# Kernel tuning notes

Measured on AMD Instinct MI355X. Metric: run time of the kernel, lower is better.

## Reference

```python
import jax, jax.numpy as jnp
import numpy as np

C = 8            # feat_channel
B, K, H, W = 8, 32, 128, 128
CW = (C + 2) * C + C + C * C + C + C + 1  # 169


def setup_inputs() -> dict:
    key = jax.random.key(0)
    k1, k2, k3, k4, k5 = jax.random.split(key, 5)
    seg_feat = jax.random.normal(k1, (B, C, H, W), jnp.float32)
    conv_weight = jax.random.normal(k2, (B, CW, H, W), jnp.float32) * 0.1
    mask = jax.random.randint(k3, (B, K), 0, 2).astype(jnp.int32)
    ind = jax.random.randint(k4, (B, K), 0, H * W).astype(jnp.int64)
    target = jax.random.uniform(k5, (B, K, H, W), jnp.float32)
    return {"seg_feat": seg_feat, "conv_weight": conv_weight, "mask": mask,
            "ind": ind, "target": target}


def reference(seg_feat, conv_weight, mask, ind, target):
    b, c, h, w = seg_feat.shape
    k = ind.shape[1]
    # gather_feature(conv_weight, ind, use_transform=True): [B,CW,H,W] -> [B,HW,CW] -> gather -> [B,K,CW]
    cw = conv_weight.reshape(b, -1, h * w).transpose(0, 2, 1)
    weight = jnp.take_along_axis(cw, ind[:, :, None], axis=1)  # [B,K,CW]

    sizes = [(c + 2) * c, c, c * c, c, c, 1]
    splits = np.cumsum(sizes)[:-1]
    c1w, c1b, c2w, c2b, c3w, c3b = jnp.split(weight, splits, axis=-1)
    c1w = c1w.reshape(b, k, c, c + 2)   # per-object 1x1 conv weights
    c2w = c2w.reshape(b, k, c, c)
    c3w = c3w.reshape(b, k, 1, c)

    x = (ind % w).astype(jnp.float32)
    y = (ind // w).astype(jnp.float32)
    y_grid, x_grid = jnp.meshgrid(jnp.arange(h, dtype=jnp.float32),
                                  jnp.arange(w, dtype=jnp.float32), indexing='ij')
    x_rel = (x_grid[None, None] - x[:, :, None, None]) / w   # [B,K,H,W]
    y_rel = (y_grid[None, None] - y[:, :, None, None]) / h

    feat = jnp.concatenate([
        jnp.broadcast_to(seg_feat[:, None], (b, k, c, h, w)),
        x_rel[:, :, None], y_rel[:, :, None]], axis=2)       # [B,K,C+2,H,W]

    feat = jax.nn.relu(jnp.einsum('bkoc,bkchw->bkohw', c1w, feat) + c1b[..., None, None])
    feat = jax.nn.relu(jnp.einsum('bkoc,bkchw->bkohw', c2w, feat) + c2b[..., None, None])
    pred = jax.nn.sigmoid(jnp.einsum('bkoc,bkchw->bkohw', c3w, feat)
                          + c3b[..., None, None])[:, :, 0]    # [B,K,H,W]

    m = mask.astype(jnp.float32)[:, :, None, None]
    p = pred * m
    t = target * m
    smooth = 1.0
    inter = jnp.sum(p * t, axis=(1, 2, 3))
    denom = jnp.sum(p * p, axis=(1, 2, 3)) + jnp.sum(t * t, axis=(1, 2, 3)) + smooth
    per_img = 1.0 - (2.0 * inter + smooth) / denom
    return jnp.mean(per_img)   # sum over images / valid_batch_size (all valid)
```

## Files before the change

### kernel.cpp

```cpp
#include <hip/hip_runtime.h>

#define C8     8
#define KOBJ   32
#define BIMG   8
#define WW     128
#define HH     128
#define HWPIX  16384
#define CWN    169
#define GRIDX  16
#define PIX    4
#define NBLK_PER_B (KOBJ * GRIDX)


__global__ __launch_bounds__(256) void mask_head_kernel(
    const float* __restrict__ seg_feat,
    const float* __restrict__ conv_weight,
    const int* __restrict__ mask,
    const long long* __restrict__ ind,
    const float* __restrict__ target,
    float* __restrict__ partial)
{
    const int b    = blockIdx.z;
    const int k    = blockIdx.y;
    const int tile = blockIdx.x;
    const int t    = threadIdx.x;
    const int blockFlat = (b * KOBJ + k) * GRIDX + tile;
    float* my = partial + blockFlat * 3;

    if (mask[b * KOBJ + k] == 0) {
        if (t == 0) { my[0] = 0.f; my[1] = 0.f; my[2] = 0.f; }
        return;
    }

    __shared__ float w[CWN];
    __shared__ float red[4][3];

    const int idx = (int)ind[b * KOBJ + k];
    if (t < CWN) {
        w[t] = conv_weight[(b * CWN + t) * HWPIX + idx];
    }
    __syncthreads();

    const float cx = (float)(idx & (WW - 1));
    const float cy = (float)(idx >> 7);

    const float* seg = seg_feat + b * C8 * HWPIX;
    const float* tgt = target + (b * KOBJ + k) * HWPIX;

    const int p0 = tile * (256 * PIX) + t;

    float sx[PIX], sy[PIX];
#pragma unroll
    for (int i = 0; i < PIX; ++i) {
        const int p = p0 + i * 256;
        sx[i] = ((float)(p & (WW - 1)) - cx) * (1.0f / 128.0f);
        sy[i] = ((float)(p >> 7)       - cy) * (1.0f / 128.0f);
    }

    float f[C8][PIX];
#pragma unroll
    for (int c = 0; c < C8; ++c)
#pragma unroll
        for (int i = 0; i < PIX; ++i)
            f[c][i] = seg[c * HWPIX + p0 + i * 256];

    float h1[C8][PIX];
#pragma unroll
    for (int o = 0; o < C8; ++o) {
        float acc[PIX];
        const float bias = w[80 + o];
#pragma unroll
        for (int i = 0; i < PIX; ++i) acc[i] = bias;
#pragma unroll
        for (int c = 0; c < C8; ++c) {
            const float wv = w[o * 10 + c];
#pragma unroll
            for (int i = 0; i < PIX; ++i) acc[i] = fmaf(wv, f[c][i], acc[i]);
        }
        const float wx = w[o * 10 + 8];
        const float wy = w[o * 10 + 9];
#pragma unroll
        for (int i = 0; i < PIX; ++i) {
            acc[i] = fmaf(wx, sx[i], acc[i]);
            acc[i] = fmaf(wy, sy[i], acc[i]);
            h1[o][i] = fmaxf(acc[i], 0.f);
        }
    }

    float h2[C8][PIX];
#pragma unroll
    for (int o = 0; o < C8; ++o) {
        float acc[PIX];
        const float bias = w[152 + o];
#pragma unroll
        for (int i = 0; i < PIX; ++i) acc[i] = bias;
#pragma unroll
        for (int c = 0; c < C8; ++c) {
            const float wv = w[88 + o * 8 + c];
#pragma unroll
            for (int i = 0; i < PIX; ++i) acc[i] = fmaf(wv, h1[c][i], acc[i]);
        }
#pragma unroll
        for (int i = 0; i < PIX; ++i) h2[o][i] = fmaxf(acc[i], 0.f);
    }

    float z[PIX];
    const float b3 = w[168];
#pragma unroll
    for (int i = 0; i < PIX; ++i) z[i] = b3;
#pragma unroll
    for (int c = 0; c < C8; ++c) {
        const float wv = w[160 + c];
#pragma unroll
        for (int i = 0; i < PIX; ++i) z[i] = fmaf(wv, h2[c][i], z[i]);
    }

    float s_pt = 0.f, s_pp = 0.f, s_tt = 0.f;
#pragma unroll
    for (int i = 0; i < PIX; ++i) {
        const float pred = 1.0f / (1.0f + __expf(-z[i]));
        const float tv   = tgt[p0 + i * 256];
        s_pt = fmaf(pred, tv, s_pt);
        s_pp = fmaf(pred, pred, s_pp);
        s_tt = fmaf(tv, tv, s_tt);
    }

#pragma unroll
    for (int off = 32; off > 0; off >>= 1) {
        s_pt += __shfl_down(s_pt, off);
        s_pp += __shfl_down(s_pp, off);
        s_tt += __shfl_down(s_tt, off);
    }
    const int wid = t >> 6;
    if ((t & 63) == 0) { red[wid][0] = s_pt; red[wid][1] = s_pp; red[wid][2] = s_tt; }
    __syncthreads();
    if (t == 0) {
        float a = 0.f, b2 = 0.f, c2 = 0.f;
#pragma unroll
        for (int i = 0; i < 4; ++i) { a += red[i][0]; b2 += red[i][1]; c2 += red[i][2]; }
        my[0] = a; my[1] = b2; my[2] = c2;
    }
}

__global__ __launch_bounds__(512) void finalize_kernel(
    const float* __restrict__ partial, float* __restrict__ out)
{
    const int t    = threadIdx.x;
    const int b    = t >> 6;
    const int lane = t & 63;

    float pt = 0.f, pp = 0.f, tt = 0.f;
    for (int e = lane; e < NBLK_PER_B; e += 64) {
        const float* q = partial + (b * NBLK_PER_B + e) * 3;
        pt += q[0]; pp += q[1]; tt += q[2];
    }
#pragma unroll
    for (int off = 32; off > 0; off >>= 1) {
        pt += __shfl_down(pt, off);
        pp += __shfl_down(pp, off);
        tt += __shfl_down(tt, off);
    }
    __shared__ float per[BIMG];
    if (lane == 0) {
        per[b] = 1.0f - (2.0f * pt + 1.0f) / (pp + tt + 1.0f);
    }
    __syncthreads();
    if (t == 0) {
        float s = 0.f;
#pragma unroll
        for (int i = 0; i < BIMG; ++i) s += per[i];
        out[0] = s * (1.0f / (float)BIMG);
    }
}

extern "C" void kernel_launch(void* const* d_in, const int* in_sizes, int n_in,
                              void* d_out, int out_size, void* d_ws, size_t ws_size,
                              hipStream_t stream) {
    const float*     seg  = (const float*)d_in[0];
    const float*     cw   = (const float*)d_in[1];
    const int*       mask = (const int*)d_in[2];
    const long long* ind  = (const long long*)d_in[3];
    const float*     tgt  = (const float*)d_in[4];
    float* out     = (float*)d_out;
    float* partial = (float*)d_ws;

    dim3 grid(GRIDX, KOBJ, BIMG);
    mask_head_kernel<<<grid, 256, 0, stream>>>(seg, cw, mask, ind, tgt, partial);
    finalize_kernel<<<1, 512, 0, stream>>>(partial, out);
}
```

Measured before the change: 20.82 us.

## Vectorize pixel loads, pack weights in aligned LDS, double pixels per thread

```diff
diff --git a/kernel.cpp b/kernel.cpp
--- a/kernel.cpp
+++ b/kernel.cpp
@@ -7,8 +7,8 @@
 #define HH     128
 #define HWPIX  16384
 #define CWN    169
-#define GRIDX  16
-#define PIX    4
+#define PIX    8
+#define GRIDX  8
 #define NBLK_PER_B (KOBJ * GRIDX)
 
 
@@ -32,12 +32,23 @@
         return;
     }
 
-    __shared__ float w[CWN];
+    __shared__ __align__(16) float l1w[C8][12];
+    __shared__ __align__(16) float l2w[C8][C8];
+    __shared__ __align__(16) float l1b[C8];
+    __shared__ __align__(16) float l2b[C8];
+    __shared__ __align__(16) float l3w[C8];
+    __shared__ float l3b_s;
     __shared__ float red[4][3];
 
     const int idx = (int)ind[b * KOBJ + k];
     if (t < CWN) {
-        w[t] = conv_weight[(b * CWN + t) * HWPIX + idx];
+        const float v = conv_weight[(b * CWN + t) * HWPIX + idx];
+        if (t < 80)       { l1w[t / 10][t % 10] = v; }
+        else if (t < 88)  { l1b[t - 80] = v; }
+        else if (t < 152) { const int u = t - 88; l2w[u >> 3][u & 7] = v; }
+        else if (t < 160) { l2b[t - 152] = v; }
+        else if (t < 168) { l3w[t - 160] = v; }
+        else              { l3b_s = v; }
     }
     __syncthreads();
 
@@ -47,82 +58,93 @@
     const float* seg = seg_feat + b * C8 * HWPIX;
     const float* tgt = target + (b * KOBJ + k) * HWPIX;
 
-    const int p0 = tile * (256 * PIX) + t;
-
-    float sx[PIX], sy[PIX];
+    const int p0 = (tile * 256 + t) * PIX;
+
+    const float4 t4a = *reinterpret_cast<const float4*>(&tgt[p0]);
+    const float4 t4b = *reinterpret_cast<const float4*>(&tgt[p0 + 4]);
+
+    const float sy  = ((float)(p0 >> 7) - cy) * (1.0f / 128.0f);
+    const float sx0 = ((float)(p0 & (WW - 1)) - cx) * (1.0f / 128.0f);
+    float sx[PIX];
+#pragma unroll
+    for (int i = 0; i < PIX; ++i) sx[i] = sx0 + (float)i * (1.0f / 128.0f);
+
+    float f[C8][PIX];
+#pragma unroll
+    for (int c = 0; c < C8; ++c) {
+        const float4 a = *reinterpret_cast<const float4*>(&seg[c * HWPIX + p0]);
+        const float4 d = *reinterpret_cast<const float4*>(&seg[c * HWPIX + p0 + 4]);
+        f[c][0] = a.x; f[c][1] = a.y; f[c][2] = a.z; f[c][3] = a.w;
+        f[c][4] = d.x; f[c][5] = d.y; f[c][6] = d.z; f[c][7] = d.w;
+    }
+
+    float h1[C8][PIX];
+#pragma unroll
+    for (int o = 0; o < C8; ++o) {
+        const float4 wa = *reinterpret_cast<const float4*>(&l1w[o][0]);
+        const float4 wb = *reinterpret_cast<const float4*>(&l1w[o][4]);
+        const float4 wc = *reinterpret_cast<const float4*>(&l1w[o][8]);
+        const float base = fmaf(wc.y, sy, l1b[o]);
+#pragma unroll
+        for (int i = 0; i < PIX; ++i) {
+            float a = fmaf(wc.x, sx[i], base);
+            a = fmaf(wa.x, f[0][i], a);
+            a = fmaf(wa.y, f[1][i], a);
+            a = fmaf(wa.z, f[2][i], a);
+            a = fmaf(wa.w, f[3][i], a);
+            a = fmaf(wb.x, f[4][i], a);
+            a = fmaf(wb.y, f[5][i], a);
+            a = fmaf(wb.z, f[6][i], a);
+            a = fmaf(wb.w, f[7][i], a);
+            h1[o][i] = fmaxf(a, 0.f);
+        }
+    }
+
+    float h2[C8][PIX];
+#pragma unroll
+    for (int o = 0; o < C8; ++o) {
+        const float4 wa = *reinterpret_cast<const float4*>(&l2w[o][0]);
+        const float4 wb = *reinterpret_cast<const float4*>(&l2w[o][4]);
+        const float bias = l2b[o];
+#pragma unroll
+        for (int i = 0; i < PIX; ++i) {
+            float a = bias;
+            a = fmaf(wa.x, h1[0][i], a);
+            a = fmaf(wa.y, h1[1][i], a);
+            a = fmaf(wa.z, h1[2][i], a);
+            a = fmaf(wa.w, h1[3][i], a);
+            a = fmaf(wb.x, h1[4][i], a);
+            a = fmaf(wb.y, h1[5][i], a);
+            a = fmaf(wb.z, h1[6][i], a);
+            a = fmaf(wb.w, h1[7][i], a);
+            h2[o][i] = fmaxf(a, 0.f);
+        }
+    }
+
+    const float4 wa = *reinterpret_cast<const float4*>(&l3w[0]);
+    const float4 wb = *reinterpret_cast<const float4*>(&l3w[4]);
+    const float b3 = l3b_s;
+    float tv[PIX];
+    tv[0] = t4a.x; tv[1] = t4a.y; tv[2] = t4a.z; tv[3] = t4a.w;
+    tv[4] = t4b.x; tv[5] = t4b.y; tv[6] = t4b.z; tv[7] = t4b.w;
+
+    float s_pt = 0.f, s_pp = 0.f, s_tt = 0.f;
 #pragma unroll
     for (int i = 0; i < PIX; ++i) {
-        const int p = p0 + i * 256;
-        sx[i] = ((float)(p & (WW - 1)) - cx) * (1.0f / 128.0f);
-        sy[i] = ((float)(p >> 7)       - cy) * (1.0f / 128.0f);
-    }
-
-    float f[C8][PIX];
-#pragma unroll
-    for (int c = 0; c < C8; ++c)
-#pragma unroll
-        for (int i = 0; i < PIX; ++i)
-            f[c][i] = seg[c * HWPIX + p0 + i * 256];
-
-    float h1[C8][PIX];
-#pragma unroll
-    for (int o = 0; o < C8; ++o) {
-        float acc[PIX];
-        const float bias = w[80 + o];
-#pragma unroll
-        for (int i = 0; i < PIX; ++i) acc[i] = bias;
-#pragma unroll
-        for (int c = 0; c < C8; ++c) {
-            const float wv = w[o * 10 + c];
-#pragma unroll
-            for (int i = 0; i < PIX; ++i) acc[i] = fmaf(wv, f[c][i], acc[i]);
-        }
-        const float wx = w[o * 10 + 8];
-        const float wy = w[o * 10 + 9];
-#pragma unroll
-        for (int i = 0; i < PIX; ++i) {
-            acc[i] = fmaf(wx, sx[i], acc[i]);
-            acc[i] = fmaf(wy, sy[i], acc[i]);
-            h1[o][i] = fmaxf(acc[i], 0.f);
-        }
-    }
-
-    float h2[C8][PIX];
-#pragma unroll
-    for (int o = 0; o < C8; ++o) {
-        float acc[PIX];
-        const float bias = w[152 + o];
-#pragma unroll
-        for (int i = 0; i < PIX; ++i) acc[i] = bias;
-#pragma unroll
-        for (int c = 0; c < C8; ++c) {
-            const float wv = w[88 + o * 8 + c];
-#pragma unroll
-            for (int i = 0; i < PIX; ++i) acc[i] = fmaf(wv, h1[c][i], acc[i]);
-        }
-#pragma unroll
-        for (int i = 0; i < PIX; ++i) h2[o][i] = fmaxf(acc[i], 0.f);
-    }
-
-    float z[PIX];
-    const float b3 = w[168];
-#pragma unroll
-    for (int i = 0; i < PIX; ++i) z[i] = b3;
-#pragma unroll
-    for (int c = 0; c < C8; ++c) {
-        const float wv = w[160 + c];
-#pragma unroll
-        for (int i = 0; i < PIX; ++i) z[i] = fmaf(wv, h2[c][i], z[i]);
-    }
-
-    float s_pt = 0.f, s_pp = 0.f, s_tt = 0.f;
-#pragma unroll
-    for (int i = 0; i < PIX; ++i) {
-        const float pred = 1.0f / (1.0f + __expf(-z[i]));
-        const float tv   = tgt[p0 + i * 256];
-        s_pt = fmaf(pred, tv, s_pt);
+        float z = b3;
+        z = fmaf(wa.x, h2[0][i], z);
+        z = fmaf(wa.y, h2[1][i], z);
+        z = fmaf(wa.z, h2[2][i], z);
+        z = fmaf(wa.w, h2[3][i], z);
+        z = fmaf(wb.x, h2[4][i], z);
+        z = fmaf(wb.y, h2[5][i], z);
+        z = fmaf(wb.z, h2[6][i], z);
+        z = fmaf(wb.w, h2[7][i], z);
+        const float e    = __expf(-z);
+        const float pred = __builtin_amdgcn_rcpf(1.0f + e);
+        s_pt = fmaf(pred, tv[i], s_pt);
         s_pp = fmaf(pred, pred, s_pp);
-        s_tt = fmaf(tv, tv, s_tt);
+        s_tt = fmaf(tv[i], tv[i], s_tt);
     }
 
 #pragma unroll
```

New measurement: 19.73 us. -5.2%, faster.

## Compact active objects to low block ids, vectorize loads, use packed FMA

Applied to the files above, without the earlier changes.

```diff
diff --git a/kernel.cpp b/kernel.cpp
--- a/kernel.cpp
+++ b/kernel.cpp
@@ -1,16 +1,22 @@
 #include <hip/hip_runtime.h>
+
+typedef float f32x2 __attribute__((ext_vector_type(2)));
 
 #define C8     8
 #define KOBJ   32
 #define BIMG   8
 #define WW     128
-#define HH     128
 #define HWPIX  16384
 #define CWN    169
-#define GRIDX  16
-#define PIX    4
-#define NBLK_PER_B (KOBJ * GRIDX)
-
+#define PIX    8
+#define GRIDX  8
+#define NPAIR  (BIMG * KOBJ)
+#define SLOTS_PER_B (KOBJ * GRIDX)
+#define NBLK   (NPAIR * GRIDX)
+
+__device__ __forceinline__ void pkfma(f32x2& d, f32x2 a, f32x2 b) {
+    asm("v_pk_fma_f32 %0, %1, %2, %0" : "+v"(d) : "v"(a), "v"(b));
+}
 
 __global__ __launch_bounds__(256) void mask_head_kernel(
     const float* __restrict__ seg_feat,
@@ -20,24 +26,71 @@
     const float* __restrict__ target,
     float* __restrict__ partial)
 {
-    const int b    = blockIdx.z;
-    const int k    = blockIdx.y;
-    const int tile = blockIdx.x;
+    const int j    = blockIdx.x;
+    const int r    = j >> 3;
+    const int tile = j & 7;
     const int t    = threadIdx.x;
-    const int blockFlat = (b * KOBJ + k) * GRIDX + tile;
-    float* my = partial + blockFlat * 3;
-
-    if (mask[b * KOBJ + k] == 0) {
-        if (t == 0) { my[0] = 0.f; my[1] = 0.f; my[2] = 0.f; }
+
+    __shared__ f32x2 wd1[C8][10];
+    __shared__ f32x2 l1b2[C8];
+    __shared__ f32x2 wd2[C8][C8];
+    __shared__ f32x2 l2b2[C8];
+    __shared__ f32x2 w3d[C8];
+    __shared__ float b3s;
+    __shared__ float red[4][3];
+    __shared__ int   sh_pair, sh_active;
+
+    if (t < 64) {
+        const int lane = t;
+        const int4 mv = *reinterpret_cast<const int4*>(&mask[lane * 4]);
+        const int a0 = (mv.x != 0), a1 = (mv.y != 0), a2 = (mv.z != 0), a3 = (mv.w != 0);
+        const int c0 = a0 + a1 + a2 + a3;
+        int incl = c0;
+#pragma unroll
+        for (int off = 1; off < 64; off <<= 1) {
+            const int n = __shfl_up(incl, off);
+            if (lane >= off) incl += n;
+        }
+        const int excl  = incl - c0;
+        const int total = __shfl(incl, 63);
+        const int use_act = (r < total) ? 1 : 0;
+        const int rr   = use_act ? r : (r - total);
+        const int base = use_act ? excl : (4 * lane - excl);
+        const int cnt  = use_act ? c0 : (4 - c0);
+        const bool has = (rr >= base) && (rr < base + cnt);
+        const int w0 = use_act ? a0 : 1 - a0;
+        const int w1 = use_act ? a1 : 1 - a1;
+        const int w2 = use_act ? a2 : 1 - a2;
+        const int d  = rr - base;
+        const int s0 = w0, s1 = w0 + w1, s2 = w0 + w1 + w2;
+        const int off4 = (d < s0) ? 0 : (d < s1) ? 1 : (d < s2) ? 2 : 3;
+        const int pcand = lane * 4 + off4;
+        const unsigned long long bal = __ballot(has);
+        const int src = (int)__ffsll((long long)bal) - 1;
+        const int pv = __shfl(pcand, src);
+        if (lane == 0) { sh_pair = pv; sh_active = use_act; }
+    }
+    __syncthreads();
+
+    const int pair = sh_pair;
+    const int slot = pair * GRIDX + tile;
+    if (!sh_active) {
+        if (t < 3) partial[slot * 3 + t] = 0.f;
         return;
     }
 
-    __shared__ float w[CWN];
-    __shared__ float red[4][3];
-
-    const int idx = (int)ind[b * KOBJ + k];
+    const int b = pair >> 5;
+    const int idx = (int)ind[pair];
+
     if (t < CWN) {
-        w[t] = conv_weight[(b * CWN + t) * HWPIX + idx];
+        const float v = conv_weight[(b * CWN + t) * HWPIX + idx];
+        const f32x2 v2 = {v, v};
+        if (t < 80)       { wd1[t / 10][t % 10] = v2; }
+        else if (t < 88)  { l1b2[t - 80] = v2; }
+        else if (t < 152) { const int u = t - 88; wd2[u >> 3][u & 7] = v2; }
+        else if (t < 160) { l2b2[t - 152] = v2; }
+        else if (t < 168) { w3d[t - 160] = v2; }
+        else              { b3s = v; }
     }
     __syncthreads();
 
@@ -45,84 +98,82 @@
     const float cy = (float)(idx >> 7);
 
     const float* seg = seg_feat + b * C8 * HWPIX;
-    const float* tgt = target + (b * KOBJ + k) * HWPIX;
-
-    const int p0 = tile * (256 * PIX) + t;
-
-    float sx[PIX], sy[PIX];
-#pragma unroll
-    for (int i = 0; i < PIX; ++i) {
-        const int p = p0 + i * 256;
-        sx[i] = ((float)(p & (WW - 1)) - cx) * (1.0f / 128.0f);
-        sy[i] = ((float)(p >> 7)       - cy) * (1.0f / 128.0f);
-    }
-
-    float f[C8][PIX];
-#pragma unroll
-    for (int c = 0; c < C8; ++c)
-#pragma unroll
-        for (int i = 0; i < PIX; ++i)
-            f[c][i] = seg[c * HWPIX + p0 + i * 256];
-
-    float h1[C8][PIX];
-#pragma unroll
-    for (int o = 0; o < C8; ++o) {
-        float acc[PIX];
-        const float bias = w[80 + o];
-#pragma unroll
-        for (int i = 0; i < PIX; ++i) acc[i] = bias;
+    const float* tgt = target + pair * HWPIX;
+
+    const int p0   = tile * 2048 + t * PIX;
+    const int row  = p0 >> 7;
+    const int col0 = p0 & (WW - 1);
+    const float sy = ((float)row - cy) * (1.0f / 128.0f);
+    const f32x2 sy2 = {sy, sy};
+
+    const float4 tA = *reinterpret_cast<const float4*>(&tgt[p0]);
+    const float4 tB = *reinterpret_cast<const float4*>(&tgt[p0 + 4]);
+
+    float s_pt = 0.f, s_pp = 0.f, s_tt = 0.f;
+
+#pragma unroll
+    for (int h = 0; h < 2; ++h) {
+        const int q = p0 + h * 4;
+        const float colq = (float)(col0 + h * 4);
+        const f32x2 sxa = {(colq - cx) * (1.0f / 128.0f),
+                           (colq + 1.0f - cx) * (1.0f / 128.0f)};
+        const f32x2 sxb = {(colq + 2.0f - cx) * (1.0f / 128.0f),
+                           (colq + 3.0f - cx) * (1.0f / 128.0f)};
+
+        f32x2 f2[C8][2];
 #pragma unroll
         for (int c = 0; c < C8; ++c) {
-            const float wv = w[o * 10 + c];
-#pragma unroll
-            for (int i = 0; i < PIX; ++i) acc[i] = fmaf(wv, f[c][i], acc[i]);
-        }
-        const float wx = w[o * 10 + 8];
-        const float wy = w[o * 10 + 9];
-#pragma unroll
-        for (int i = 0; i < PIX; ++i) {
-            acc[i] = fmaf(wx, sx[i], acc[i]);
-            acc[i] = fmaf(wy, sy[i], acc[i]);
-            h1[o][i] = fmaxf(acc[i], 0.f);
-        }
-    }
-
-    float h2[C8][PIX];
-#pragma unroll
-    for (int o = 0; o < C8; ++o) {
-        float acc[PIX];
-        const float bias = w[152 + o];
-#pragma unroll
-        for (int i = 0; i < PIX; ++i) acc[i] = bias;
-#pragma unroll
-        for (int c = 0; c < C8; ++c) {
-            const float wv = w[88 + o * 8 + c];
-#pragma unroll
-            for (int i = 0; i < PIX; ++i) acc[i] = fmaf(wv, h1[c][i], acc[i]);
-        }
-#pragma unroll
-        for (int i = 0; i < PIX; ++i) h2[o][i] = fmaxf(acc[i], 0.f);
-    }
-
-    float z[PIX];
-    const float b3 = w[168];
-#pragma unroll
-    for (int i = 0; i < PIX; ++i) z[i] = b3;
-#pragma unroll
-    for (int c = 0; c < C8; ++c) {
-        const float wv = w[160 + c];
-#pragma unroll
-        for (int i = 0; i < PIX; ++i) z[i] = fmaf(wv, h2[c][i], z[i]);
-    }
-
-    float s_pt = 0.f, s_pp = 0.f, s_tt = 0.f;
-#pragma unroll
-    for (int i = 0; i < PIX; ++i) {
-        const float pred = 1.0f / (1.0f + __expf(-z[i]));
-        const float tv   = tgt[p0 + i * 256];
-        s_pt = fmaf(pred, tv, s_pt);
-        s_pp = fmaf(pred, pred, s_pp);
-        s_tt = fmaf(tv, tv, s_tt);
+            const float4 a = *reinterpret_cast<const float4*>(&seg[c * HWPIX + q]);
+            f2[c][0] = {a.x, a.y};
+            f2[c][1] = {a.z, a.w};
+        }
+
+        f32x2 h1[C8][2];
+#pragma unroll
+        for (int o = 0; o < C8; ++o) {
+            f32x2 base2 = l1b2[o];
+            pkfma(base2, wd1[o][9], sy2);
+            f32x2 acc0 = base2, acc1 = base2;
+            pkfma(acc0, wd1[o][8], sxa);
+            pkfma(acc1, wd1[o][8], sxb);
+#pragma unroll
+            for (int c = 0; c < C8; ++c) {
+                const f32x2 w = wd1[o][c];
+                pkfma(acc0, w, f2[c][0]);
+                pkfma(acc1, w, f2[c][1]);
+            }
+            h1[o][0] = {fmaxf(acc0.x, 0.f), fmaxf(acc0.y, 0.f)};
+            h1[o][1] = {fmaxf(acc1.x, 0.f), fmaxf(acc1.y, 0.f)};
+        }
+
+        f32x2 z0 = {b3s, b3s}, z1 = z0;
+#pragma unroll
+        for (int o = 0; o < C8; ++o) {
+            f32x2 acc0 = l2b2[o], acc1 = l2b2[o];
+#pragma unroll
+            for (int c = 0; c < C8; ++c) {
+                const f32x2 w = wd2[o][c];
+                pkfma(acc0, w, h1[c][0]);
+                pkfma(acc1, w, h1[c][1]);
+            }
+            const f32x2 r0 = {fmaxf(acc0.x, 0.f), fmaxf(acc0.y, 0.f)};
+            const f32x2 r1 = {fmaxf(acc1.x, 0.f), fmaxf(acc1.y, 0.f)};
+            const f32x2 w3 = w3d[o];
+            pkfma(z0, w3, r0);
+            pkfma(z1, w3, r1);
+        }
+
+        const float zz[4] = {z0.x, z0.y, z1.x, z1.y};
+        const float4 tq = (h == 0) ? tA : tB;
+        const float tv[4] = {tq.x, tq.y, tq.z, tq.w};
+#pragma unroll
+        for (int i = 0; i < 4; ++i) {
+            const float e    = __expf(-zz[i]);
+            const float pred = __builtin_amdgcn_rcpf(1.0f + e);
+            s_pt = fmaf(pred, tv[i], s_pt);
+            s_pp = fmaf(pred, pred, s_pp);
+            s_tt = fmaf(tv[i], tv[i], s_tt);
+        }
     }
 
 #pragma unroll
@@ -138,7 +189,9 @@
         float a = 0.f, b2 = 0.f, c2 = 0.f;
 #pragma unroll
         for (int i = 0; i < 4; ++i) { a += red[i][0]; b2 += red[i][1]; c2 += red[i][2]; }
-        my[0] = a; my[1] = b2; my[2] = c2;
+        partial[slot * 3 + 0] = a;
+        partial[slot * 3 + 1] = b2;
+        partial[slot * 3 + 2] = c2;
     }
 }
 
@@ -150,8 +203,8 @@
     const int lane = t & 63;
 
     float pt = 0.f, pp = 0.f, tt = 0.f;
-    for (int e = lane; e < NBLK_PER_B; e += 64) {
-        const float* q = partial + (b * NBLK_PER_B + e) * 3;
+    for (int e = lane; e < SLOTS_PER_B; e += 64) {
+        const float* q = partial + (b * SLOTS_PER_B + e) * 3;
         pt += q[0]; pp += q[1]; tt += q[2];
     }
 #pragma unroll
@@ -184,7 +237,6 @@
     float* out     = (float*)d_out;
     float* partial = (float*)d_ws;
 
-    dim3 grid(GRIDX, KOBJ, BIMG);
-    mask_head_kernel<<<grid, 256, 0, stream>>>(seg, cw, mask, ind, tgt, partial);
+    mask_head_kernel<<<dim3(NBLK), 256, 0, stream>>>(seg, cw, mask, ind, tgt, partial);
     finalize_kernel<<<1, 512, 0, stream>>>(partial, out);
 }
```

New measurement: 21.02 us. No clear change (+0.9%).

## Vectorize pixel loads, drop block syncs with per-wave weight copies and partials

Applied to the files above, without the earlier changes.

```diff
diff --git a/kernel.cpp b/kernel.cpp
--- a/kernel.cpp
+++ b/kernel.cpp
@@ -4,12 +4,12 @@
 #define KOBJ   32
 #define BIMG   8
 #define WW     128
-#define HH     128
 #define HWPIX  16384
 #define CWN    169
-#define GRIDX  16
-#define PIX    4
-#define NBLK_PER_B (KOBJ * GRIDX)
+#define PIX    8
+#define GRIDX  8
+#define NBLK   (BIMG * KOBJ * GRIDX)
+#define WSLOTS_PER_B (KOBJ * GRIDX * 4)
 
 
 __global__ __launch_bounds__(256) void mask_head_kernel(
@@ -20,109 +20,122 @@
     const float* __restrict__ target,
     float* __restrict__ partial)
 {
+    const int tile = blockIdx.x;
+    const int k    = blockIdx.y;
     const int b    = blockIdx.z;
-    const int k    = blockIdx.y;
-    const int tile = blockIdx.x;
     const int t    = threadIdx.x;
-    const int blockFlat = (b * KOBJ + k) * GRIDX + tile;
-    float* my = partial + blockFlat * 3;
+    const int lane = t & 63;
+    const int wid  = t >> 6;
+    const int pair = b * KOBJ + k;
+    const int slot = pair * GRIDX + tile;
+    float* wout = partial + (slot * 4 + wid) * 3;
 
-    if (mask[b * KOBJ + k] == 0) {
-        if (t == 0) { my[0] = 0.f; my[1] = 0.f; my[2] = 0.f; }
+    const int       mval  = mask[pair];
+    const long long idxll = ind[pair];
+    if (mval == 0) {
+        if (lane == 0) { wout[0] = 0.f; wout[1] = 0.f; wout[2] = 0.f; }
         return;
     }
+    const int idx = (int)idxll;
 
-    __shared__ float w[CWN];
-    __shared__ float red[4][3];
+    __shared__ float wds[4][CWN + 7];
+    float* wp = wds[wid];
 
-    const int idx = (int)ind[b * KOBJ + k];
-    if (t < CWN) {
-        w[t] = conv_weight[(b * CWN + t) * HWPIX + idx];
-    }
-    __syncthreads();
+    const float* cwb = conv_weight + b * CWN * HWPIX + idx;
+    const float g0 = cwb[lane * HWPIX];
+    const float g1 = cwb[(lane + 64) * HWPIX];
+    float g2 = 0.f;
+    if (lane < CWN - 128) g2 = cwb[(lane + 128) * HWPIX];
+
+    const float* seg = seg_feat + b * C8 * HWPIX;
+    const float* tgt = target + pair * HWPIX;
+    const int p0   = tile * 2048 + t * PIX;
+    const float4 tA = *reinterpret_cast<const float4*>(&tgt[p0]);
+    const float4 tB = *reinterpret_cast<const float4*>(&tgt[p0 + 4]);
+    float4 s0[C8];
+#pragma unroll
+    for (int c = 0; c < C8; ++c)
+        s0[c] = *reinterpret_cast<const float4*>(&seg[c * HWPIX + p0]);
+
+    wp[lane] = g0;
+    wp[lane + 64] = g1;
+    if (lane < CWN - 128) wp[lane + 128] = g2;
 
     const float cx = (float)(idx & (WW - 1));
     const float cy = (float)(idx >> 7);
+    const int row  = p0 >> 7;
+    const int col0 = p0 & (WW - 1);
+    const float sy = ((float)row - cy) * (1.0f / 128.0f);
+    float sx[PIX];
+#pragma unroll
+    for (int i = 0; i < PIX; ++i)
+        sx[i] = ((float)(col0 + i) - cx) * (1.0f / 128.0f);
 
-    const float* seg = seg_feat + b * C8 * HWPIX;
-    const float* tgt = target + (b * KOBJ + k) * HWPIX;
+    float s_pt = 0.f, s_pp = 0.f, s_tt = 0.f;
 
-    const int p0 = tile * (256 * PIX) + t;
+#pragma unroll
+    for (int h = 0; h < 2; ++h) {
+        float f[C8][4];
+        if (h == 0) {
+#pragma unroll
+            for (int c = 0; c < C8; ++c) {
+                f[c][0] = s0[c].x; f[c][1] = s0[c].y;
+                f[c][2] = s0[c].z; f[c][3] = s0[c].w;
+            }
+        } else {
+#pragma unroll
+            for (int c = 0; c < C8; ++c) {
+                const float4 a = *reinterpret_cast<const float4*>(&seg[c * HWPIX + p0 + 4]);
+                f[c][0] = a.x; f[c][1] = a.y; f[c][2] = a.z; f[c][3] = a.w;
+            }
+        }
 
-    float sx[PIX], sy[PIX];
+        float h1[C8][4];
 #pragma unroll
-    for (int i = 0; i < PIX; ++i) {
-        const int p = p0 + i * 256;
-        sx[i] = ((float)(p & (WW - 1)) - cx) * (1.0f / 128.0f);
-        sy[i] = ((float)(p >> 7)       - cy) * (1.0f / 128.0f);
-    }
+        for (int o = 0; o < C8; ++o) {
+            const float wx = wp[o * 10 + 8];
+            const float wy = wp[o * 10 + 9];
+            const float base = fmaf(wy, sy, wp[80 + o]);
+#pragma unroll
+            for (int i = 0; i < 4; ++i) {
+                float a = fmaf(wx, sx[h * 4 + i], base);
+#pragma unroll
+                for (int c = 0; c < C8; ++c)
+                    a = fmaf(wp[o * 10 + c], f[c][i], a);
+                h1[o][i] = fmaxf(a, 0.f);
+            }
+        }
 
-    float f[C8][PIX];
+        float z[4];
+        {
+            const float b3 = wp[168];
 #pragma unroll
-    for (int c = 0; c < C8; ++c)
-#pragma unroll
-        for (int i = 0; i < PIX; ++i)
-            f[c][i] = seg[c * HWPIX + p0 + i * 256];
-
-    float h1[C8][PIX];
-#pragma unroll
-    for (int o = 0; o < C8; ++o) {
-        float acc[PIX];
-        const float bias = w[80 + o];
-#pragma unroll
-        for (int i = 0; i < PIX; ++i) acc[i] = bias;
-#pragma unroll
-        for (int c = 0; c < C8; ++c) {
-            const float wv = w[o * 10 + c];
-#pragma unroll
-            for (int i = 0; i < PIX; ++i) acc[i] = fmaf(wv, f[c][i], acc[i]);
-        }
-        const float wx = w[o * 10 + 8];
-        const float wy = w[o * 10 + 9];
-#pragma unroll
-        for (int i = 0; i < PIX; ++i) {
-            acc[i] = fmaf(wx, sx[i], acc[i]);
-            acc[i] = fmaf(wy, sy[i], acc[i]);
-            h1[o][i] = fmaxf(acc[i], 0.f);
-        }
-    }
-
-    float h2[C8][PIX];
-#pragma unroll
-    for (int o = 0; o < C8; ++o) {
-        float acc[PIX];
-        const float bias = w[152 + o];
-#pragma unroll
-        for (int i = 0; i < PIX; ++i) acc[i] = bias;
-#pragma unroll
-        for (int c = 0; c < C8; ++c) {
-            const float wv = w[88 + o * 8 + c];
-#pragma unroll
-            for (int i = 0; i < PIX; ++i) acc[i] = fmaf(wv, h1[c][i], acc[i]);
+            for (int i = 0; i < 4; ++i) z[i] = b3;
         }
 #pragma unroll
-        for (int i = 0; i < PIX; ++i) h2[o][i] = fmaxf(acc[i], 0.f);
-    }
+        for (int o = 0; o < C8; ++o) {
+            const float bias = wp[152 + o];
+            const float w3   = wp[160 + o];
+#pragma unroll
+            for (int i = 0; i < 4; ++i) {
+                float a = bias;
+#pragma unroll
+                for (int c = 0; c < C8; ++c)
+                    a = fmaf(wp[88 + o * 8 + c], h1[c][i], a);
+                z[i] = fmaf(w3, fmaxf(a, 0.f), z[i]);
+            }
+        }
 
-    float z[PIX];
-    const float b3 = w[168];
+        const float4 tq = (h == 0) ? tA : tB;
+        const float tv[4] = {tq.x, tq.y, tq.z, tq.w};
 #pragma unroll
-    for (int i = 0; i < PIX; ++i) z[i] = b3;
-#pragma unroll
-    for (int c = 0; c < C8; ++c) {
-        const float wv = w[160 + c];
-#pragma unroll
-        for (int i = 0; i < PIX; ++i) z[i] = fmaf(wv, h2[c][i], z[i]);
-    }
-
-    float s_pt = 0.f, s_pp = 0.f, s_tt = 0.f;
-#pragma unroll
-    for (int i = 0; i < PIX; ++i) {
-        const float pred = 1.0f / (1.0f + __expf(-z[i]));
-        const float tv   = tgt[p0 + i * 256];
-        s_pt = fmaf(pred, tv, s_pt);
-        s_pp = fmaf(pred, pred, s_pp);
-        s_tt = fmaf(tv, tv, s_tt);
+        for (int i = 0; i < 4; ++i) {
+            const float e    = __expf(-z[i]);
+            const float pred = __builtin_amdgcn_rcpf(1.0f + e);
+            s_pt = fmaf(pred, tv[i], s_pt);
+            s_pp = fmaf(pred, pred, s_pp);
+            s_tt = fmaf(tv[i], tv[i], s_tt);
+        }
     }
 
 #pragma unroll
@@ -131,15 +144,7 @@
         s_pp += __shfl_down(s_pp, off);
         s_tt += __shfl_down(s_tt, off);
     }
-    const int wid = t >> 6;
-    if ((t & 63) == 0) { red[wid][0] = s_pt; red[wid][1] = s_pp; red[wid][2] = s_tt; }
-    __syncthreads();
-    if (t == 0) {
-        float a = 0.f, b2 = 0.f, c2 = 0.f;
-#pragma unroll
-        for (int i = 0; i < 4; ++i) { a += red[i][0]; b2 += red[i][1]; c2 += red[i][2]; }
-        my[0] = a; my[1] = b2; my[2] = c2;
-    }
+    if (lane == 0) { wout[0] = s_pt; wout[1] = s_pp; wout[2] = s_tt; }
 }
 
 __global__ __launch_bounds__(512) void finalize_kernel(
@@ -150,8 +155,9 @@
     const int lane = t & 63;
 
     float pt = 0.f, pp = 0.f, tt = 0.f;
-    for (int e = lane; e < NBLK_PER_B; e += 64) {
-        const float* q = partial + (b * NBLK_PER_B + e) * 3;
+    const float* base = partial + b * WSLOTS_PER_B * 3;
+    for (int e = lane; e < WSLOTS_PER_B; e += 64) {
+        const float* q = base + e * 3;
         pt += q[0]; pp += q[1]; tt += q[2];
     }
 #pragma unroll
@@ -184,7 +190,7 @@
     float* out     = (float*)d_out;
     float* partial = (float*)d_ws;
 
-    dim3 grid(GRIDX, KOBJ, BIMG);
-    mask_head_kernel<<<grid, 256, 0, stream>>>(seg, cw, mask, ind, tgt, partial);
+    mask_head_kernel<<<dim3(GRIDX, KOBJ, BIMG), 256, 0, stream>>>(
+        seg, cw, mask, ind, tgt, partial);
     finalize_kernel<<<1, 512, 0, stream>>>(partial, out);
 }
```

New measurement: 24.42 us. 17.3% more time.
